# Kernel tuning notes

Measured on AMD Instinct MI355X. Metric: run time of the kernel, lower is better.

The kernel has to match this reference:

```python
import math
import jax, jax.numpy as jnp
import numpy as np

GROUPS = 32
EPS = 1e-5


def group_norm(x, w, b):
    # x: [B, C, H, W]
    B, C, H, W = x.shape
    xg = x.reshape(B, GROUPS, C // GROUPS, H, W)
    mean = xg.mean(axis=(2, 3, 4), keepdims=True)
    var = xg.var(axis=(2, 3, 4), keepdims=True)
    xg = (xg - mean) * jax.lax.rsqrt(var + EPS)
    x = xg.reshape(B, C, H, W)
    return x * w[None, :, None, None] + b[None, :, None, None]


def setup_inputs() -> dict:
    key = jax.random.key(0)
    ks = jax.random.split(key, 4)
    B, C, H, W = 16, 512, 32, 32
    x = jax.random.normal(ks[0], (B, C, H, W), dtype=jnp.float32)
    norm_w = jnp.ones((C,), dtype=jnp.float32)
    norm_b = jnp.zeros((C,), dtype=jnp.float32)
    qkv_w = jax.random.normal(ks[1], (3 * C, C), dtype=jnp.float32) / math.sqrt(C)
    qkv_b = jnp.zeros((3 * C,), dtype=jnp.float32)
    proj_w = jax.random.normal(ks[2], (C, C), dtype=jnp.float32) / math.sqrt(C)
    proj_b = jnp.zeros((C,), dtype=jnp.float32)
    return {"x": x, "norm_w": norm_w, "norm_b": norm_b,
            "qkv_w": qkv_w, "qkv_b": qkv_b,
            "proj_w": proj_w, "proj_b": proj_b}


def reference(x, norm_w, norm_b, qkv_w, qkv_b, proj_w, proj_b):
    B, C, H, W = x.shape
    xn = group_norm(x, norm_w, norm_b)
    # 1x1 conv == channel matmul: [B,3C,H,W]
    qkv = jnp.einsum('oc,bchw->bohw', qkv_w, xn) + qkv_b[None, :, None, None]
    q, k, v = jnp.split(qkv, 3, axis=1)
    q = q.reshape(B, C, H * W).transpose(0, 2, 1)  # [B, HW, C]
    k = k.reshape(B, C, H * W)                     # [B, C, HW]
    v = v.reshape(B, C, H * W).transpose(0, 2, 1)  # [B, HW, C]
    attn = jax.nn.softmax(jnp.einsum('bnc,bcm->bnm', q, k) / math.sqrt(C), axis=-1)
    h = jnp.einsum('bnm,bmc->bnc', attn, v)        # [B, HW, C]
    h = h.transpose(0, 2, 1).reshape(B, C, H, W)
    out = jnp.einsum('oc,bchw->bohw', proj_w, h) + proj_b[None, :, None, None]
    return out + x
```

## Files before the change

kernel.cpp:

```cpp
#include <hip/hip_runtime.h>

#define GLD16(gp, lp) __builtin_amdgcn_global_load_lds( \
    (const __attribute__((address_space(1))) void*)(gp), \
    (__attribute__((address_space(3))) void*)(lp), 16, 0, 0)

typedef __attribute__((ext_vector_type(8))) short bf16x8;
typedef __attribute__((ext_vector_type(4))) float f32x4;

__device__ __forceinline__ short f2bf(float f) {
    union { float f; unsigned u; } x; x.f = f;
    unsigned r = x.u + 0x7fffu + ((x.u >> 16) & 1u);
    return (short)(r >> 16);
}
__device__ __forceinline__ float bf2f(short s) {
    union { unsigned u; float f; } x;
    x.u = ((unsigned)(unsigned short)s) << 16;
    return x.f;
}

__global__ __launch_bounds__(256) void cvt_weights(
    const float* __restrict__ qkv_w, const float* __restrict__ proj_w,
    short* __restrict__ wq, short* __restrict__ wp)
{
    int idx = blockIdx.x * 256 + threadIdx.x;
    const int NQ4 = (1536 * 512) / 4;
    float4 f; short4 s;
    if (idx < NQ4) {
        f = ((const float4*)qkv_w)[idx];
        s.x = f2bf(f.x); s.y = f2bf(f.y); s.z = f2bf(f.z); s.w = f2bf(f.w);
        ((short4*)wq)[idx] = s;
    } else {
        int j = idx - NQ4;
        f = ((const float4*)proj_w)[j];
        s.x = f2bf(f.x); s.y = f2bf(f.y); s.z = f2bf(f.z); s.w = f2bf(f.w);
        ((short4*)wp)[j] = s;
    }
}

__global__ __launch_bounds__(256) void gn_stats(
    const float* __restrict__ x, float* __restrict__ mean, float* __restrict__ rstd)
{
    int bg = blockIdx.x;
    const float4* p = (const float4*)(x + (size_t)bg * 16384);
    float s = 0.f, ss = 0.f;
    for (int i = threadIdx.x; i < 4096; i += 256) {
        float4 v = p[i];
        s  += v.x + v.y + v.z + v.w;
        ss += v.x * v.x + v.y * v.y + v.z * v.z + v.w * v.w;
    }
    #pragma unroll
    for (int o = 32; o > 0; o >>= 1) {
        s  += __shfl_down(s, o);
        ss += __shfl_down(ss, o);
    }
    __shared__ float ls[4], lss[4];
    int wave = threadIdx.x >> 6;
    if ((threadIdx.x & 63) == 0) { ls[wave] = s; lss[wave] = ss; }
    __syncthreads();
    if (threadIdx.x == 0) {
        s  = ls[0] + ls[1] + ls[2] + ls[3];
        ss = lss[0] + lss[1] + lss[2] + lss[3];
        float m = s * (1.f / 16384.f);
        float var = ss * (1.f / 16384.f) - m * m;
        mean[bg] = m;
        rstd[bg] = rsqrtf(var + 1e-5f);
    }
}

__global__ __launch_bounds__(256) void gn_apply_t(
    const float* __restrict__ x, const float* __restrict__ w, const float* __restrict__ bb,
    const float* __restrict__ mean, const float* __restrict__ rstd,
    short* __restrict__ xnT)
{
    __shared__ short tile[64][65];
    int b = blockIdx.z, cblk = blockIdx.y, nblk = blockIdx.x;
    int t = threadIdx.x;
    int nl = t & 63;
    int cb = t >> 6;
    #pragma unroll
    for (int i = 0; i < 16; ++i) {
        int cl = cb * 16 + i;
        int cg = cblk * 64 + cl;
        int bgid = b * 32 + (cg >> 4);
        float sc = rstd[bgid] * w[cg];
        float sh = bb[cg] - mean[bgid] * sc;
        float xv = x[((size_t)(b * 512 + cg)) * 1024 + nblk * 64 + nl];
        tile[cl][nl] = f2bf(xv * sc + sh);
    }
    __syncthreads();
    int ng = t >> 4;
    int c4 = (t & 15) * 4;
    #pragma unroll
    for (int p = 0; p < 4; ++p) {
        int nl2 = p * 16 + ng;
        short4 sv;
        sv.x = tile[c4 + 0][nl2];
        sv.y = tile[c4 + 1][nl2];
        sv.z = tile[c4 + 2][nl2];
        sv.w = tile[c4 + 3][nl2];
        *(short4*)&xnT[((size_t)(b * 1024 + nblk * 64 + nl2)) * 512 + cblk * 64 + c4] = sv;
    }
}

__device__ __forceinline__ void gemm256(
    const short* __restrict__ A, const short* __restrict__ B,
    const int lda, const int ldb, const int NT,
    short* lds, f32x4 acc[8][4])
{
    const int tid  = threadIdx.x;
    const int lane = tid & 63;
    const int wave = tid >> 6;
    const int wm = wave >> 2;
    const int wn = wave & 3;
    const int fr = lane & 15;
    const int fk = lane >> 4;
    const int frx = fr & 7;

    const short* pa[4]; const short* pb[4];
    int la[4], lb[4];
    #pragma unroll
    for (int i = 0; i < 4; ++i) {
        int cid = i * 512 + tid;
        int row = cid >> 3;
        int sl  = cid & 7;
        int csw = sl ^ (row & 7);
        pa[i] = A + (size_t)row * lda + csw * 8;
        pb[i] = B + (size_t)row * ldb + csw * 8;
        la[i] = cid * 8;
        lb[i] = 16384 + cid * 8;
    }

    #pragma unroll
    for (int i = 0; i < 4; ++i) GLD16(pa[i], lds + la[i]);
    #pragma unroll
    for (int i = 0; i < 4; ++i) GLD16(pb[i], lds + lb[i]);
    #pragma unroll
    for (int i = 0; i < 4; ++i) { pa[i] += 64; pb[i] += 64; }

    const int arow0 = wm * 128 + fr;
    const int brow0 = wn * 64 + fr;
    const int slot0 = (fk ^ frx) << 3;
    const int slot1 = ((4 + fk) ^ frx) << 3;

    for (int t = 0; t < NT; ++t) {
        const int cur = (t & 1) << 15;
        const int nxt = 32768 - cur;
        const bool pre = (t + 1 < NT);

        if (pre) {
            #pragma unroll
            for (int i = 0; i < 4; ++i) GLD16(pa[i], lds + nxt + la[i]);
        }
        if (pre) asm volatile("s_waitcnt vmcnt(4)" ::: "memory");
        else     asm volatile("s_waitcnt vmcnt(0)" ::: "memory");
        asm volatile("s_barrier" ::: "memory");
        __builtin_amdgcn_sched_barrier(0);

        bf16x8 af[8], bfr[4];
        #pragma unroll
        for (int m = 0; m < 8; ++m)
            af[m] = *(const bf16x8*)&lds[cur + ((arow0 + m * 16) << 6) + slot0];
        #pragma unroll
        for (int n = 0; n < 4; ++n)
            bfr[n] = *(const bf16x8*)&lds[cur + 16384 + ((brow0 + n * 16) << 6) + slot0];
        if (pre) {
            #pragma unroll
            for (int i = 0; i < 4; ++i) GLD16(pb[i], lds + nxt + lb[i]);
        }
        __builtin_amdgcn_s_setprio(1);
        #pragma unroll
        for (int m = 0; m < 8; ++m)
            #pragma unroll
            for (int n = 0; n < 4; ++n)
                acc[m][n] = __builtin_amdgcn_mfma_f32_16x16x32_bf16(af[m], bfr[n], acc[m][n], 0, 0, 0);
        __builtin_amdgcn_s_setprio(0);

        #pragma unroll
        for (int m = 0; m < 8; ++m)
            af[m] = *(const bf16x8*)&lds[cur + ((arow0 + m * 16) << 6) + slot1];
        #pragma unroll
        for (int n = 0; n < 4; ++n)
            bfr[n] = *(const bf16x8*)&lds[cur + 16384 + ((brow0 + n * 16) << 6) + slot1];
        __builtin_amdgcn_s_setprio(1);
        #pragma unroll
        for (int m = 0; m < 8; ++m)
            #pragma unroll
            for (int n = 0; n < 4; ++n)
                acc[m][n] = __builtin_amdgcn_mfma_f32_16x16x32_bf16(af[m], bfr[n], acc[m][n], 0, 0, 0);
        __builtin_amdgcn_s_setprio(0);

        if (pre) {
            #pragma unroll
            for (int i = 0; i < 4; ++i) { pa[i] += 64; pb[i] += 64; }
        }
        asm volatile("s_barrier" ::: "memory");
        __builtin_amdgcn_sched_barrier(0);
    }
}

#define GEMM_EPI_IDX() \
    const int lane = threadIdx.x & 63; \
    const int wave = threadIdx.x >> 6; \
    const int wm = wave >> 2; \
    const int wn = wave & 3; \
    const int fq = lane >> 4; \
    const int fcol = lane & 15;

__global__ __launch_bounds__(512, 2) void qkv_gemm(
    const short* __restrict__ wq, const float* __restrict__ qkv_b,
    const short* __restrict__ xnT,
    short* __restrict__ qT, short* __restrict__ kT, short* __restrict__ vv)
{
    __shared__ short lds[65536];
    const int b = blockIdx.z, bm = blockIdx.y, bn = blockIdx.x;
    const short* A  = wq + (size_t)bm * 256 * 512;
    const short* Bb = xnT + ((size_t)b * 1024 + bn * 256) * 512;
    f32x4 acc[8][4];
    #pragma unroll
    for (int m = 0; m < 8; ++m)
        #pragma unroll
        for (int n = 0; n < 4; ++n) acc[m][n] = (f32x4){0.f, 0.f, 0.f, 0.f};
    gemm256(A, Bb, 512, 512, 8, lds, acc);

    GEMM_EPI_IDX();
    const int region = bm >> 1;
    const float qscale = 0.04419417382415922f;

    #pragma unroll
    for (int m = 0; m < 8; ++m) {
        int o0 = bm * 256 + wm * 128 + m * 16 + fq * 4;
        float4 bias = *(const float4*)&qkv_b[o0];
        float bb4[4] = {bias.x, bias.y, bias.z, bias.w};
        #pragma unroll
        for (int n = 0; n < 4; ++n) {
            int col = bn * 256 + wn * 64 + n * 16 + fcol;
            f32x4 a = acc[m][n];
            if (region == 0) {
                short4 sv;
                sv.x = f2bf((a[0] + bb4[0]) * qscale);
                sv.y = f2bf((a[1] + bb4[1]) * qscale);
                sv.z = f2bf((a[2] + bb4[2]) * qscale);
                sv.w = f2bf((a[3] + bb4[3]) * qscale);
                *(short4*)&qT[((size_t)(b * 1024 + col)) * 512 + o0] = sv;
            } else if (region == 1) {
                short4 sv;
                sv.x = f2bf(a[0] + bb4[0]);
                sv.y = f2bf(a[1] + bb4[1]);
                sv.z = f2bf(a[2] + bb4[2]);
                sv.w = f2bf(a[3] + bb4[3]);
                *(short4*)&kT[((size_t)(b * 1024 + col)) * 512 + (o0 - 512)] = sv;
            } else {
                #pragma unroll
                for (int r = 0; r < 4; ++r)
                    vv[((size_t)(b * 512 + (o0 - 1024 + r))) * 1024 + col] = f2bf(a[r] + bb4[r]);
            }
        }
    }
}

__global__ __launch_bounds__(512, 2) void s_gemm(
    const short* __restrict__ kT, const short* __restrict__ qT, short* __restrict__ S)
{
    __shared__ short lds[65536];
    const int b = blockIdx.z, bm = blockIdx.y, bn = blockIdx.x;
    const short* A  = kT + ((size_t)b * 1024 + bm * 256) * 512;
    const short* Bb = qT + ((size_t)b * 1024 + bn * 256) * 512;
    f32x4 acc[8][4];
    #pragma unroll
    for (int m = 0; m < 8; ++m)
        #pragma unroll
        for (int n = 0; n < 4; ++n) acc[m][n] = (f32x4){0.f, 0.f, 0.f, 0.f};
    gemm256(A, Bb, 512, 512, 8, lds, acc);

    GEMM_EPI_IDX();
    #pragma unroll
    for (int m = 0; m < 8; ++m) {
        int m0 = bm * 256 + wm * 128 + m * 16 + fq * 4;
        #pragma unroll
        for (int n = 0; n < 4; ++n) {
            int ncol = bn * 256 + wn * 64 + n * 16 + fcol;
            f32x4 a = acc[m][n];
            short4 sv;
            sv.x = f2bf(a[0]); sv.y = f2bf(a[1]); sv.z = f2bf(a[2]); sv.w = f2bf(a[3]);
            *(short4*)&S[((size_t)(b * 1024 + ncol)) * 1024 + m0] = sv;
        }
    }
}

__global__ __launch_bounds__(256) void softmax_rows(short* __restrict__ S)
{
    const int wave = threadIdx.x >> 6;
    const int lane = threadIdx.x & 63;
    size_t row = (size_t)blockIdx.x * 4 + wave;
    short* p = S + row * 1024;
    short4 raw[4];
    float v[16];
    #pragma unroll
    for (int i = 0; i < 4; ++i) raw[i] = ((short4*)p)[lane + 64 * i];
    #pragma unroll
    for (int i = 0; i < 4; ++i) {
        v[i * 4 + 0] = bf2f(raw[i].x);
        v[i * 4 + 1] = bf2f(raw[i].y);
        v[i * 4 + 2] = bf2f(raw[i].z);
        v[i * 4 + 3] = bf2f(raw[i].w);
    }
    float mx = v[0];
    #pragma unroll
    for (int i = 1; i < 16; ++i) mx = fmaxf(mx, v[i]);
    #pragma unroll
    for (int o = 1; o < 64; o <<= 1) mx = fmaxf(mx, __shfl_xor(mx, o));
    float sum = 0.f;
    #pragma unroll
    for (int i = 0; i < 16; ++i) { v[i] = __expf(v[i] - mx); sum += v[i]; }
    #pragma unroll
    for (int o = 1; o < 64; o <<= 1) sum += __shfl_xor(sum, o);
    float inv = 1.f / sum;
    #pragma unroll
    for (int i = 0; i < 4; ++i) {
        short4 sv;
        sv.x = f2bf(v[i * 4 + 0] * inv);
        sv.y = f2bf(v[i * 4 + 1] * inv);
        sv.z = f2bf(v[i * 4 + 2] * inv);
        sv.w = f2bf(v[i * 4 + 3] * inv);
        ((short4*)p)[lane + 64 * i] = sv;
    }
}

__global__ __launch_bounds__(512, 2) void pv_gemm(
    const short* __restrict__ vv, const short* __restrict__ P, short* __restrict__ h)
{
    __shared__ short lds[65536];
    const int b = blockIdx.z, bm = blockIdx.y, bn = blockIdx.x;
    const short* A  = vv + ((size_t)b * 512 + bm * 256) * 1024;
    const short* Bb = P + ((size_t)b * 1024 + bn * 256) * 1024;
    f32x4 acc[8][4];
    #pragma unroll
    for (int m = 0; m < 8; ++m)
        #pragma unroll
        for (int n = 0; n < 4; ++n) acc[m][n] = (f32x4){0.f, 0.f, 0.f, 0.f};
    gemm256(A, Bb, 1024, 1024, 16, lds, acc);

    GEMM_EPI_IDX();
    #pragma unroll
    for (int m = 0; m < 8; ++m) {
        int c0 = bm * 256 + wm * 128 + m * 16 + fq * 4;
        #pragma unroll
        for (int n = 0; n < 4; ++n) {
            int ncol = bn * 256 + wn * 64 + n * 16 + fcol;
            f32x4 a = acc[m][n];
            short4 sv;
            sv.x = f2bf(a[0]); sv.y = f2bf(a[1]); sv.z = f2bf(a[2]); sv.w = f2bf(a[3]);
            *(short4*)&h[((size_t)(b * 1024 + ncol)) * 512 + c0] = sv;
        }
    }
}

__global__ __launch_bounds__(512, 2) void proj_gemm(
    const short* __restrict__ wp, const float* __restrict__ proj_b,
    const short* __restrict__ h, const float* __restrict__ x, float* __restrict__ out)
{
    __shared__ short lds[65536];
    const int b = blockIdx.z, bm = blockIdx.y, bn = blockIdx.x;
    const short* A  = wp + (size_t)bm * 256 * 512;
    const short* Bb = h + ((size_t)b * 1024 + bn * 256) * 512;
    f32x4 acc[8][4];
    #pragma unroll
    for (int m = 0; m < 8; ++m)
        #pragma unroll
        for (int n = 0; n < 4; ++n) acc[m][n] = (f32x4){0.f, 0.f, 0.f, 0.f};
    gemm256(A, Bb, 512, 512, 8, lds, acc);

    GEMM_EPI_IDX();
    #pragma unroll
    for (int m = 0; m < 8; ++m) {
        int o0 = bm * 256 + wm * 128 + m * 16 + fq * 4;
        float4 pb = *(const float4*)&proj_b[o0];
        float pb4[4] = {pb.x, pb.y, pb.z, pb.w};
        #pragma unroll
        for (int n = 0; n < 4; ++n) {
            int col = bn * 256 + wn * 64 + n * 16 + fcol;
            f32x4 a = acc[m][n];
            #pragma unroll
            for (int r = 0; r < 4; ++r) {
                size_t idx = ((size_t)(b * 512 + o0 + r)) * 1024 + col;
                out[idx] = a[r] + pb4[r] + x[idx];
            }
        }
    }
}

extern "C" void kernel_launch(void* const* d_in, const int* in_sizes, int n_in,
                              void* d_out, int out_size, void* d_ws, size_t ws_size,
                              hipStream_t stream) {
    const float* x      = (const float*)d_in[0];
    const float* norm_w = (const float*)d_in[1];
    const float* norm_b = (const float*)d_in[2];
    const float* qkv_w  = (const float*)d_in[3];
    const float* qkv_b  = (const float*)d_in[4];
    const float* proj_w = (const float*)d_in[5];
    const float* proj_b = (const float*)d_in[6];
    float* out = (float*)d_out;

    char* ws = (char*)d_ws;
    size_t off = 0;
    auto alloc = [&](size_t bytes) {
        void* p = ws + off;
        off = (off + bytes + 255) & ~(size_t)255;
        return p;
    };
    float* mean = (float*)alloc(512 * 4);
    float* rstd = (float*)alloc(512 * 4);
    short* wq   = (short*)alloc((size_t)1536 * 512 * 2);
    short* wp   = (short*)alloc((size_t)512 * 512 * 2);
    short* xnT  = (short*)alloc((size_t)16 * 1024 * 512 * 2);
    short* qT   = (short*)alloc((size_t)16 * 1024 * 512 * 2);
    short* kT   = (short*)alloc((size_t)16 * 1024 * 512 * 2);
    short* vv   = (short*)alloc((size_t)16 * 512 * 1024 * 2);
    short* S    = (short*)alloc((size_t)16 * 1024 * 1024 * 2);
    short* h    = xnT;

    cvt_weights<<<1024, 256, 0, stream>>>(qkv_w, proj_w, wq, wp);
    gn_stats<<<512, 256, 0, stream>>>(x, mean, rstd);
    gn_apply_t<<<dim3(16, 8, 16), 256, 0, stream>>>(x, norm_w, norm_b, mean, rstd, xnT);
    qkv_gemm<<<dim3(4, 6, 16), 512, 0, stream>>>(wq, qkv_b, xnT, qT, kT, vv);
    s_gemm<<<dim3(4, 4, 16), 512, 0, stream>>>(kT, qT, S);
    softmax_rows<<<4096, 256, 0, stream>>>(S);
    pv_gemm<<<dim3(4, 2, 16), 512, 0, stream>>>(vv, S, h);
    proj_gemm<<<dim3(4, 2, 16), 512, 0, stream>>>(wp, proj_b, h, x, out);
}
```

Measured before the change: 247.3 us.

## Use 4-stage K=32 LDS pipeline and narrower N tiles for PV/proj GEMMs

Replaces the double-buffered K=64 GEMM mainloop with a templated 4-buffer pipeline using K=32 slices. It keeps three stages in flight, needs one barrier per iteration, and uses a new swizzle for 32-wide rows. PV and projection GEMMs switch to 128-wide N tiles with twice as many blocks, which should improve CU occupancy across 256 CUs. The cost is more loop iterations, more LDS fragment loads per MFMA, and a smaller tile that re-reads the A operand more often.

```diff
diff --git a/kernel.cpp b/kernel.cpp
--- a/kernel.cpp
+++ b/kernel.cpp
@@ -102,11 +102,14 @@
     }
 }
 
-__device__ __forceinline__ void gemm256(
+template<int NFR, int NT>
+__device__ __forceinline__ void gemm_core(
     const short* __restrict__ A, const short* __restrict__ B,
-    const int lda, const int ldb, const int NT,
-    short* lds, f32x4 acc[8][4])
-{
+    const int lda, const int ldb, short* lds, f32x4 acc[8][NFR])
+{
+    constexpr int BCH = NFR / 2;
+    constexpr int BUF = 8192 + NFR * 2048;
+    constexpr int LPS = 2 + BCH;
     const int tid  = threadIdx.x;
     const int lane = tid & 63;
     const int wave = tid >> 6;
@@ -114,104 +117,82 @@
     const int wn = wave & 3;
     const int fr = lane & 15;
     const int fk = lane >> 4;
-    const int frx = fr & 7;
-
-    const short* pa[4]; const short* pb[4];
-    int la[4], lb[4];
-    #pragma unroll
-    for (int i = 0; i < 4; ++i) {
+
+    const short* pa[2]; int la[2];
+    const short* pb[BCH]; int lb[BCH];
+    #pragma unroll
+    for (int i = 0; i < 2; ++i) {
         int cid = i * 512 + tid;
-        int row = cid >> 3;
-        int sl  = cid & 7;
-        int csw = sl ^ (row & 7);
+        int row = cid >> 2, sl = cid & 3;
+        int csw = sl ^ ((row >> 1) & 3);
         pa[i] = A + (size_t)row * lda + csw * 8;
+        la[i] = cid * 8;
+    }
+    #pragma unroll
+    for (int i = 0; i < BCH; ++i) {
+        int cid = i * 512 + tid;
+        int row = cid >> 2, sl = cid & 3;
+        int csw = sl ^ ((row >> 1) & 3);
         pb[i] = B + (size_t)row * ldb + csw * 8;
-        la[i] = cid * 8;
-        lb[i] = 16384 + cid * 8;
-    }
-
-    #pragma unroll
-    for (int i = 0; i < 4; ++i) GLD16(pa[i], lds + la[i]);
-    #pragma unroll
-    for (int i = 0; i < 4; ++i) GLD16(pb[i], lds + lb[i]);
-    #pragma unroll
-    for (int i = 0; i < 4; ++i) { pa[i] += 64; pb[i] += 64; }
+        lb[i] = 8192 + cid * 8;
+    }
+
+    auto stage = [&](int t) {
+        const int base = (t & 3) * BUF;
+        const int koff = t * 32;
+        #pragma unroll
+        for (int i = 0; i < 2; ++i) GLD16(pa[i] + koff, lds + base + la[i]);
+        #pragma unroll
+        for (int i = 0; i < BCH; ++i) GLD16(pb[i] + koff, lds + base + lb[i]);
+    };
+
+    stage(0); stage(1); stage(2);
+    asm volatile("s_waitcnt vmcnt(%0)" :: "n"(2 * LPS) : "memory");
+    asm volatile("s_barrier" ::: "memory");
 
     const int arow0 = wm * 128 + fr;
-    const int brow0 = wn * 64 + fr;
-    const int slot0 = (fk ^ frx) << 3;
-    const int slot1 = ((4 + fk) ^ frx) << 3;
+    const int brow0 = wn * (NFR * 16) + fr;
 
     for (int t = 0; t < NT; ++t) {
-        const int cur = (t & 1) << 15;
-        const int nxt = 32768 - cur;
-        const bool pre = (t + 1 < NT);
-
-        if (pre) {
-            #pragma unroll
-            for (int i = 0; i < 4; ++i) GLD16(pa[i], lds + nxt + la[i]);
-        }
-        if (pre) asm volatile("s_waitcnt vmcnt(4)" ::: "memory");
-        else     asm volatile("s_waitcnt vmcnt(0)" ::: "memory");
-        asm volatile("s_barrier" ::: "memory");
-        __builtin_amdgcn_sched_barrier(0);
-
-        bf16x8 af[8], bfr[4];
-        #pragma unroll
-        for (int m = 0; m < 8; ++m)
-            af[m] = *(const bf16x8*)&lds[cur + ((arow0 + m * 16) << 6) + slot0];
-        #pragma unroll
-        for (int n = 0; n < 4; ++n)
-            bfr[n] = *(const bf16x8*)&lds[cur + 16384 + ((brow0 + n * 16) << 6) + slot0];
-        if (pre) {
-            #pragma unroll
-            for (int i = 0; i < 4; ++i) GLD16(pb[i], lds + nxt + lb[i]);
+        const int base = (t & 3) * BUF;
+        bf16x8 af[8], bfr[NFR];
+        #pragma unroll
+        for (int m = 0; m < 8; ++m) {
+            int R = arow0 + m * 16;
+            af[m] = *(const bf16x8*)&lds[base + R * 32 + ((fk ^ ((R >> 1) & 3)) << 3)];
+        }
+        #pragma unroll
+        for (int n = 0; n < NFR; ++n) {
+            int R = brow0 + n * 16;
+            bfr[n] = *(const bf16x8*)&lds[base + 8192 + R * 32 + ((fk ^ ((R >> 1) & 3)) << 3)];
         }
         __builtin_amdgcn_s_setprio(1);
         #pragma unroll
         for (int m = 0; m < 8; ++m)
             #pragma unroll
-            for (int n = 0; n < 4; ++n)
+            for (int n = 0; n < NFR; ++n)
                 acc[m][n] = __builtin_amdgcn_mfma_f32_16x16x32_bf16(af[m], bfr[n], acc[m][n], 0, 0, 0);
         __builtin_amdgcn_s_setprio(0);
 
-        #pragma unroll
-        for (int m = 0; m < 8; ++m)
-            af[m] = *(const bf16x8*)&lds[cur + ((arow0 + m * 16) << 6) + slot1];
-        #pragma unroll
-        for (int n = 0; n < 4; ++n)
-            bfr[n] = *(const bf16x8*)&lds[cur + 16384 + ((brow0 + n * 16) << 6) + slot1];
-        __builtin_amdgcn_s_setprio(1);
-        #pragma unroll
-        for (int m = 0; m < 8; ++m)
-            #pragma unroll
-            for (int n = 0; n < 4; ++n)
-                acc[m][n] = __builtin_amdgcn_mfma_f32_16x16x32_bf16(af[m], bfr[n], acc[m][n], 0, 0, 0);
-        __builtin_amdgcn_s_setprio(0);
-
-        if (pre) {
-            #pragma unroll
-            for (int i = 0; i < 4; ++i) { pa[i] += 64; pb[i] += 64; }
-        }
-        asm volatile("s_barrier" ::: "memory");
-        __builtin_amdgcn_sched_barrier(0);
-    }
-}
-
-#define GEMM_EPI_IDX() \
-    const int lane = threadIdx.x & 63; \
-    const int wave = threadIdx.x >> 6; \
-    const int wm = wave >> 2; \
-    const int wn = wave & 3; \
-    const int fq = lane >> 4; \
-    const int fcol = lane & 15;
+        if (t + 3 < NT) stage(t + 3);
+        if (t + 1 < NT) {
+            if (t + 3 < NT)
+                asm volatile("s_waitcnt vmcnt(%0)" :: "n"(2 * LPS) : "memory");
+            else if (t + 2 < NT)
+                asm volatile("s_waitcnt vmcnt(%0)" :: "n"(LPS) : "memory");
+            else
+                asm volatile("s_waitcnt vmcnt(0)" ::: "memory");
+            asm volatile("s_barrier" ::: "memory");
+        }
+    }
+}
 
 __global__ __launch_bounds__(512, 2) void qkv_gemm(
     const short* __restrict__ wq, const float* __restrict__ qkv_b,
     const short* __restrict__ xnT,
     short* __restrict__ qT, short* __restrict__ kT, short* __restrict__ vv)
 {
-    __shared__ short lds[65536];
+    __shared__ short lds[4 * (8192 + 4 * 2048)];
     const int b = blockIdx.z, bm = blockIdx.y, bn = blockIdx.x;
     const short* A  = wq + (size_t)bm * 256 * 512;
     const short* Bb = xnT + ((size_t)b * 1024 + bn * 256) * 512;
@@ -220,9 +201,12 @@
     for (int m = 0; m < 8; ++m)
         #pragma unroll
         for (int n = 0; n < 4; ++n) acc[m][n] = (f32x4){0.f, 0.f, 0.f, 0.f};
-    gemm256(A, Bb, 512, 512, 8, lds, acc);
-
-    GEMM_EPI_IDX();
+    gemm_core<4, 16>(A, Bb, 512, 512, lds, acc);
+
+    const int lane = threadIdx.x & 63;
+    const int wave = threadIdx.x >> 6;
+    const int wm = wave >> 2, wn = wave & 3;
+    const int fq = lane >> 4, fcol = lane & 15;
     const int region = bm >> 1;
     const float qscale = 0.04419417382415922f;
 
@@ -261,7 +245,7 @@
 __global__ __launch_bounds__(512, 2) void s_gemm(
     const short* __restrict__ kT, const short* __restrict__ qT, short* __restrict__ S)
 {
-    __shared__ short lds[65536];
+    __shared__ short lds[4 * (8192 + 4 * 2048)];
     const int b = blockIdx.z, bm = blockIdx.y, bn = blockIdx.x;
     const short* A  = kT + ((size_t)b * 1024 + bm * 256) * 512;
     const short* Bb = qT + ((size_t)b * 1024 + bn * 256) * 512;
@@ -270,9 +254,12 @@
     for (int m = 0; m < 8; ++m)
         #pragma unroll
         for (int n = 0; n < 4; ++n) acc[m][n] = (f32x4){0.f, 0.f, 0.f, 0.f};
-    gemm256(A, Bb, 512, 512, 8, lds, acc);
-
-    GEMM_EPI_IDX();
+    gemm_core<4, 16>(A, Bb, 512, 512, lds, acc);
+
+    const int lane = threadIdx.x & 63;
+    const int wave = threadIdx.x >> 6;
+    const int wm = wave >> 2, wn = wave & 3;
+    const int fq = lane >> 4, fcol = lane & 15;
     #pragma unroll
     for (int m = 0; m < 8; ++m) {
         int m0 = bm * 256 + wm * 128 + m * 16 + fq * 4;
@@ -329,24 +316,27 @@
 __global__ __launch_bounds__(512, 2) void pv_gemm(
     const short* __restrict__ vv, const short* __restrict__ P, short* __restrict__ h)
 {
-    __shared__ short lds[65536];
+    __shared__ short lds[4 * (8192 + 2 * 2048)];
     const int b = blockIdx.z, bm = blockIdx.y, bn = blockIdx.x;
     const short* A  = vv + ((size_t)b * 512 + bm * 256) * 1024;
-    const short* Bb = P + ((size_t)b * 1024 + bn * 256) * 1024;
-    f32x4 acc[8][4];
+    const short* Bb = P + ((size_t)b * 1024 + bn * 128) * 1024;
+    f32x4 acc[8][2];
     #pragma unroll
     for (int m = 0; m < 8; ++m)
         #pragma unroll
-        for (int n = 0; n < 4; ++n) acc[m][n] = (f32x4){0.f, 0.f, 0.f, 0.f};
-    gemm256(A, Bb, 1024, 1024, 16, lds, acc);
-
-    GEMM_EPI_IDX();
+        for (int n = 0; n < 2; ++n) acc[m][n] = (f32x4){0.f, 0.f, 0.f, 0.f};
+    gemm_core<2, 32>(A, Bb, 1024, 1024, lds, acc);
+
+    const int lane = threadIdx.x & 63;
+    const int wave = threadIdx.x >> 6;
+    const int wm = wave >> 2, wn = wave & 3;
+    const int fq = lane >> 4, fcol = lane & 15;
     #pragma unroll
     for (int m = 0; m < 8; ++m) {
         int c0 = bm * 256 + wm * 128 + m * 16 + fq * 4;
         #pragma unroll
-        for (int n = 0; n < 4; ++n) {
-            int ncol = bn * 256 + wn * 64 + n * 16 + fcol;
+        for (int n = 0; n < 2; ++n) {
+            int ncol = bn * 128 + wn * 32 + n * 16 + fcol;
             f32x4 a = acc[m][n];
             short4 sv;
             sv.x = f2bf(a[0]); sv.y = f2bf(a[1]); sv.z = f2bf(a[2]); sv.w = f2bf(a[3]);
@@ -359,26 +349,29 @@
     const short* __restrict__ wp, const float* __restrict__ proj_b,
     const short* __restrict__ h, const float* __restrict__ x, float* __restrict__ out)
 {
-    __shared__ short lds[65536];
+    __shared__ short lds[4 * (8192 + 2 * 2048)];
     const int b = blockIdx.z, bm = blockIdx.y, bn = blockIdx.x;
     const short* A  = wp + (size_t)bm * 256 * 512;
-    const short* Bb = h + ((size_t)b * 1024 + bn * 256) * 512;
-    f32x4 acc[8][4];
+    const short* Bb = h + ((size_t)b * 1024 + bn * 128) * 512;
+    f32x4 acc[8][2];
     #pragma unroll
     for (int m = 0; m < 8; ++m)
         #pragma unroll
-        for (int n = 0; n < 4; ++n) acc[m][n] = (f32x4){0.f, 0.f, 0.f, 0.f};
-    gemm256(A, Bb, 512, 512, 8, lds, acc);
-
-    GEMM_EPI_IDX();
+        for (int n = 0; n < 2; ++n) acc[m][n] = (f32x4){0.f, 0.f, 0.f, 0.f};
+    gemm_core<2, 16>(A, Bb, 512, 512, lds, acc);
+
+    const int lane = threadIdx.x & 63;
+    const int wave = threadIdx.x >> 6;
+    const int wm = wave >> 2, wn = wave & 3;
+    const int fq = lane >> 4, fcol = lane & 15;
     #pragma unroll
     for (int m = 0; m < 8; ++m) {
         int o0 = bm * 256 + wm * 128 + m * 16 + fq * 4;
         float4 pb = *(const float4*)&proj_b[o0];
         float pb4[4] = {pb.x, pb.y, pb.z, pb.w};
         #pragma unroll
-        for (int n = 0; n < 4; ++n) {
-            int col = bn * 256 + wn * 64 + n * 16 + fcol;
+        for (int n = 0; n < 2; ++n) {
+            int col = bn * 128 + wn * 32 + n * 16 + fcol;
             f32x4 a = acc[m][n];
             #pragma unroll
             for (int r = 0; r < 4; ++r) {
@@ -425,6 +418,6 @@
     qkv_gemm<<<dim3(4, 6, 16), 512, 0, stream>>>(wq, qkv_b, xnT, qT, kT, vv);
     s_gemm<<<dim3(4, 4, 16), 512, 0, stream>>>(kT, qT, S);
     softmax_rows<<<4096, 256, 0, stream>>>(S);
-    pv_gemm<<<dim3(4, 2, 16), 512, 0, stream>>>(vv, S, h);
-    proj_gemm<<<dim3(4, 2, 16), 512, 0, stream>>>(wp, proj_b, h, x, out);
-}
+    pv_gemm<<<dim3(8, 2, 16), 512, 0, stream>>>(vv, S, h);
+    proj_gemm<<<dim3(8, 2, 16), 512, 0, stream>>>(wp, proj_b, h, x, out);
+}
```

Measured after the change: 243.1 us. About the same (-1.7%).

## Use triple-buffered K32 GEMM pipeline, XCD-aware block swizzle, and fuse prep kernels

Applied to the files above, without the earlier changes.

Rewrites the shared GEMM mainloop to use K=32 stages in a three-slot LDS ring (96KB instead of 128KB) with a new XOR swizzle. Loads are issued two stages ahead and B fragment reads are split around interleaved barriers, so global-load latency overlaps MFMA work. All GEMM launches become 1D grids remapped so that neighbouring tiles land on the same XCD, which should improve L2 reuse. Weight conversion and group-norm statistics are merged into a single launch. The cost is more barriers per K step and higher scheduling complexity.

```diff
diff --git a/kernel.cpp b/kernel.cpp
--- a/kernel.cpp
+++ b/kernel.cpp
@@ -17,53 +17,55 @@
     x.u = ((unsigned)(unsigned short)s) << 16;
     return x.f;
 }
-
-__global__ __launch_bounds__(256) void cvt_weights(
+__device__ __forceinline__ int xcd_swz(int id, int n) {
+    return (id & 7) * (n >> 3) + (id >> 3);
+}
+
+__global__ __launch_bounds__(256) void prep(
     const float* __restrict__ qkv_w, const float* __restrict__ proj_w,
-    short* __restrict__ wq, short* __restrict__ wp)
-{
-    int idx = blockIdx.x * 256 + threadIdx.x;
-    const int NQ4 = (1536 * 512) / 4;
-    float4 f; short4 s;
-    if (idx < NQ4) {
-        f = ((const float4*)qkv_w)[idx];
-        s.x = f2bf(f.x); s.y = f2bf(f.y); s.z = f2bf(f.z); s.w = f2bf(f.w);
-        ((short4*)wq)[idx] = s;
+    short* __restrict__ wq, short* __restrict__ wp,
+    const float* __restrict__ x, float* __restrict__ mean, float* __restrict__ rstd)
+{
+    if (blockIdx.x < 1024) {
+        int idx = blockIdx.x * 256 + threadIdx.x;
+        const int NQ4 = (1536 * 512) / 4;
+        float4 f; short4 s;
+        if (idx < NQ4) {
+            f = ((const float4*)qkv_w)[idx];
+            s.x = f2bf(f.x); s.y = f2bf(f.y); s.z = f2bf(f.z); s.w = f2bf(f.w);
+            ((short4*)wq)[idx] = s;
+        } else {
+            int j = idx - NQ4;
+            f = ((const float4*)proj_w)[j];
+            s.x = f2bf(f.x); s.y = f2bf(f.y); s.z = f2bf(f.z); s.w = f2bf(f.w);
+            ((short4*)wp)[j] = s;
+        }
     } else {
-        int j = idx - NQ4;
-        f = ((const float4*)proj_w)[j];
-        s.x = f2bf(f.x); s.y = f2bf(f.y); s.z = f2bf(f.z); s.w = f2bf(f.w);
-        ((short4*)wp)[j] = s;
-    }
-}
-
-__global__ __launch_bounds__(256) void gn_stats(
-    const float* __restrict__ x, float* __restrict__ mean, float* __restrict__ rstd)
-{
-    int bg = blockIdx.x;
-    const float4* p = (const float4*)(x + (size_t)bg * 16384);
-    float s = 0.f, ss = 0.f;
-    for (int i = threadIdx.x; i < 4096; i += 256) {
-        float4 v = p[i];
-        s  += v.x + v.y + v.z + v.w;
-        ss += v.x * v.x + v.y * v.y + v.z * v.z + v.w * v.w;
-    }
-    #pragma unroll
-    for (int o = 32; o > 0; o >>= 1) {
-        s  += __shfl_down(s, o);
-        ss += __shfl_down(ss, o);
-    }
-    __shared__ float ls[4], lss[4];
-    int wave = threadIdx.x >> 6;
-    if ((threadIdx.x & 63) == 0) { ls[wave] = s; lss[wave] = ss; }
-    __syncthreads();
-    if (threadIdx.x == 0) {
-        s  = ls[0] + ls[1] + ls[2] + ls[3];
-        ss = lss[0] + lss[1] + lss[2] + lss[3];
-        float m = s * (1.f / 16384.f);
-        float var = ss * (1.f / 16384.f) - m * m;
-        mean[bg] = m;
-        rstd[bg] = rsqrtf(var + 1e-5f);
+        int bg = blockIdx.x - 1024;
+        const float4* p = (const float4*)(x + (size_t)bg * 16384);
+        float s = 0.f, ss = 0.f;
+        for (int i = threadIdx.x; i < 4096; i += 256) {
+            float4 v = p[i];
+            s  += v.x + v.y + v.z + v.w;
+            ss += v.x * v.x + v.y * v.y + v.z * v.z + v.w * v.w;
+        }
+        #pragma unroll
+        for (int o = 32; o > 0; o >>= 1) {
+            s  += __shfl_down(s, o);
+            ss += __shfl_down(ss, o);
+        }
+        __shared__ float ls[4], lss[4];
+        int wave = threadIdx.x >> 6;
+        if ((threadIdx.x & 63) == 0) { ls[wave] = s; lss[wave] = ss; }
+        __syncthreads();
+        if (threadIdx.x == 0) {
+            s  = ls[0] + ls[1] + ls[2] + ls[3];
+            ss = lss[0] + lss[1] + lss[2] + lss[3];
+            float m = s * (1.f / 16384.f);
+            float var = ss * (1.f / 16384.f) - m * m;
+            mean[bg] = m;
+            rstd[bg] = rsqrtf(var + 1e-5f);
+        }
     }
 }
 
@@ -102,10 +104,10 @@
     }
 }
 
-__device__ __forceinline__ void gemm256(
+template<int NT>
+__device__ __forceinline__ void gemm256_8p(
     const short* __restrict__ A, const short* __restrict__ B,
-    const int lda, const int ldb, const int NT,
-    short* lds, f32x4 acc[8][4])
+    const int lda, const int ldb, short* lds, f32x4 acc[8][4])
 {
     const int tid  = threadIdx.x;
     const int lane = tid & 63;
@@ -114,91 +116,93 @@
     const int wn = wave & 3;
     const int fr = lane & 15;
     const int fk = lane >> 4;
-    const int frx = fr & 7;
-
-    const short* pa[4]; const short* pb[4];
-    int la[4], lb[4];
-    #pragma unroll
-    for (int i = 0; i < 4; ++i) {
+
+    const short* pa[2]; const short* pb[2]; int la[2], lb[2];
+    #pragma unroll
+    for (int i = 0; i < 2; ++i) {
         int cid = i * 512 + tid;
-        int row = cid >> 3;
-        int sl  = cid & 7;
-        int csw = sl ^ (row & 7);
+        int row = cid >> 2, sl = cid & 3;
+        int csw = sl ^ ((row >> 1) & 3);
         pa[i] = A + (size_t)row * lda + csw * 8;
         pb[i] = B + (size_t)row * ldb + csw * 8;
         la[i] = cid * 8;
-        lb[i] = 16384 + cid * 8;
-    }
-
-    #pragma unroll
-    for (int i = 0; i < 4; ++i) GLD16(pa[i], lds + la[i]);
-    #pragma unroll
-    for (int i = 0; i < 4; ++i) GLD16(pb[i], lds + lb[i]);
-    #pragma unroll
-    for (int i = 0; i < 4; ++i) { pa[i] += 64; pb[i] += 64; }
+        lb[i] = 8192 + cid * 8;
+    }
+
+    #pragma unroll
+    for (int i = 0; i < 2; ++i) GLD16(pa[i],      lds + la[i]);
+    #pragma unroll
+    for (int i = 0; i < 2; ++i) GLD16(pb[i],      lds + lb[i]);
+    #pragma unroll
+    for (int i = 0; i < 2; ++i) GLD16(pa[i] + 32, lds + 16384 + la[i]);
+    #pragma unroll
+    for (int i = 0; i < 2; ++i) GLD16(pb[i] + 32, lds + 16384 + lb[i]);
+    asm volatile("s_waitcnt vmcnt(4)" ::: "memory");
+    asm volatile("s_barrier" ::: "memory");
 
     const int arow0 = wm * 128 + fr;
     const int brow0 = wn * 64 + fr;
-    const int slot0 = (fk ^ frx) << 3;
-    const int slot1 = ((4 + fk) ^ frx) << 3;
-
+
+    int base = 0, sbase = 32768, kst = 64;
     for (int t = 0; t < NT; ++t) {
-        const int cur = (t & 1) << 15;
-        const int nxt = 32768 - cur;
-        const bool pre = (t + 1 < NT);
+        const short* lA = lds + base;
+        const short* lB = lds + base + 8192;
+        const bool pre = (t + 2 < NT);
 
         if (pre) {
+            GLD16(pa[0] + kst, lds + sbase + la[0]);
+            GLD16(pa[1] + kst, lds + sbase + la[1]);
+        }
+        bf16x8 af[8], bf0[2];
+        #pragma unroll
+        for (int m = 0; m < 8; ++m) {
+            int R = arow0 + m * 16;
+            af[m] = *(const bf16x8*)&lA[R * 32 + ((fk ^ ((R >> 1) & 3)) << 3)];
+        }
+        #pragma unroll
+        for (int n = 0; n < 2; ++n) {
+            int R = brow0 + n * 16;
+            bf0[n] = *(const bf16x8*)&lB[R * 32 + ((fk ^ ((R >> 1) & 3)) << 3)];
+        }
+        asm volatile("s_barrier" ::: "memory");
+        __builtin_amdgcn_s_setprio(1);
+        #pragma unroll
+        for (int m = 0; m < 8; ++m)
             #pragma unroll
-            for (int i = 0; i < 4; ++i) GLD16(pa[i], lds + nxt + la[i]);
-        }
-        if (pre) asm volatile("s_waitcnt vmcnt(4)" ::: "memory");
-        else     asm volatile("s_waitcnt vmcnt(0)" ::: "memory");
+            for (int n = 0; n < 2; ++n)
+                acc[m][n] = __builtin_amdgcn_mfma_f32_16x16x32_bf16(af[m], bf0[n], acc[m][n], 0, 0, 0);
+        __builtin_amdgcn_s_setprio(0);
+
+        if (pre) {
+            GLD16(pb[0] + kst, lds + sbase + lb[0]);
+            GLD16(pb[1] + kst, lds + sbase + lb[1]);
+        }
+        bf16x8 bf1[2];
+        #pragma unroll
+        for (int n = 0; n < 2; ++n) {
+            int R = brow0 + (n + 2) * 16;
+            bf1[n] = *(const bf16x8*)&lB[R * 32 + ((fk ^ ((R >> 1) & 3)) << 3)];
+        }
+        asm volatile("s_barrier" ::: "memory");
+        __builtin_amdgcn_s_setprio(1);
+        #pragma unroll
+        for (int m = 0; m < 8; ++m)
+            #pragma unroll
+            for (int n = 0; n < 2; ++n)
+                acc[m][n + 2] = __builtin_amdgcn_mfma_f32_16x16x32_bf16(af[m], bf1[n], acc[m][n + 2], 0, 0, 0);
+        __builtin_amdgcn_s_setprio(0);
+
+        if (pre)                 asm volatile("s_waitcnt vmcnt(4)" ::: "memory");
+        else if (t + 1 < NT)     asm volatile("s_waitcnt vmcnt(0)" ::: "memory");
         asm volatile("s_barrier" ::: "memory");
         __builtin_amdgcn_sched_barrier(0);
-
-        bf16x8 af[8], bfr[4];
-        #pragma unroll
-        for (int m = 0; m < 8; ++m)
-            af[m] = *(const bf16x8*)&lds[cur + ((arow0 + m * 16) << 6) + slot0];
-        #pragma unroll
-        for (int n = 0; n < 4; ++n)
-            bfr[n] = *(const bf16x8*)&lds[cur + 16384 + ((brow0 + n * 16) << 6) + slot0];
-        if (pre) {
-            #pragma unroll
-            for (int i = 0; i < 4; ++i) GLD16(pb[i], lds + nxt + lb[i]);
-        }
-        __builtin_amdgcn_s_setprio(1);
-        #pragma unroll
-        for (int m = 0; m < 8; ++m)
-            #pragma unroll
-            for (int n = 0; n < 4; ++n)
-                acc[m][n] = __builtin_amdgcn_mfma_f32_16x16x32_bf16(af[m], bfr[n], acc[m][n], 0, 0, 0);
-        __builtin_amdgcn_s_setprio(0);
-
-        #pragma unroll
-        for (int m = 0; m < 8; ++m)
-            af[m] = *(const bf16x8*)&lds[cur + ((arow0 + m * 16) << 6) + slot1];
-        #pragma unroll
-        for (int n = 0; n < 4; ++n)
-            bfr[n] = *(const bf16x8*)&lds[cur + 16384 + ((brow0 + n * 16) << 6) + slot1];
-        __builtin_amdgcn_s_setprio(1);
-        #pragma unroll
-        for (int m = 0; m < 8; ++m)
-            #pragma unroll
-            for (int n = 0; n < 4; ++n)
-                acc[m][n] = __builtin_amdgcn_mfma_f32_16x16x32_bf16(af[m], bfr[n], acc[m][n], 0, 0, 0);
-        __builtin_amdgcn_s_setprio(0);
-
-        if (pre) {
-            #pragma unroll
-            for (int i = 0; i < 4; ++i) { pa[i] += 64; pb[i] += 64; }
-        }
-        asm volatile("s_barrier" ::: "memory");
-        __builtin_amdgcn_sched_barrier(0);
-    }
-}
-
-#define GEMM_EPI_IDX() \
+        base  = (base  == 32768) ? 0 : base  + 16384;
+        sbase = (sbase == 32768) ? 0 : sbase + 16384;
+        kst += 32;
+    }
+}
+
+#define EPI_IDX() \
     const int lane = threadIdx.x & 63; \
     const int wave = threadIdx.x >> 6; \
     const int wm = wave >> 2; \
@@ -211,8 +215,9 @@
     const short* __restrict__ xnT,
     short* __restrict__ qT, short* __restrict__ kT, short* __restrict__ vv)
 {
-    __shared__ short lds[65536];
-    const int b = blockIdx.z, bm = blockIdx.y, bn = blockIdx.x;
+    __shared__ short lds[49152];
+    int wg = xcd_swz(blockIdx.x, 384);
+    const int bn = wg & 3, bm = (wg >> 2) % 6, b = wg / 24;
     const short* A  = wq + (size_t)bm * 256 * 512;
     const short* Bb = xnT + ((size_t)b * 1024 + bn * 256) * 512;
     f32x4 acc[8][4];
@@ -220,9 +225,9 @@
     for (int m = 0; m < 8; ++m)
         #pragma unroll
         for (int n = 0; n < 4; ++n) acc[m][n] = (f32x4){0.f, 0.f, 0.f, 0.f};
-    gemm256(A, Bb, 512, 512, 8, lds, acc);
-
-    GEMM_EPI_IDX();
+    gemm256_8p<16>(A, Bb, 512, 512, lds, acc);
+
+    EPI_IDX();
     const int region = bm >> 1;
     const float qscale = 0.04419417382415922f;
 
@@ -261,8 +266,9 @@
 __global__ __launch_bounds__(512, 2) void s_gemm(
     const short* __restrict__ kT, const short* __restrict__ qT, short* __restrict__ S)
 {
-    __shared__ short lds[65536];
-    const int b = blockIdx.z, bm = blockIdx.y, bn = blockIdx.x;
+    __shared__ short lds[49152];
+    int wg = xcd_swz(blockIdx.x, 256);
+    const int bn = wg & 3, bm = (wg >> 2) & 3, b = wg >> 4;
     const short* A  = kT + ((size_t)b * 1024 + bm * 256) * 512;
     const short* Bb = qT + ((size_t)b * 1024 + bn * 256) * 512;
     f32x4 acc[8][4];
@@ -270,9 +276,9 @@
     for (int m = 0; m < 8; ++m)
         #pragma unroll
         for (int n = 0; n < 4; ++n) acc[m][n] = (f32x4){0.f, 0.f, 0.f, 0.f};
-    gemm256(A, Bb, 512, 512, 8, lds, acc);
-
-    GEMM_EPI_IDX();
+    gemm256_8p<16>(A, Bb, 512, 512, lds, acc);
+
+    EPI_IDX();
     #pragma unroll
     for (int m = 0; m < 8; ++m) {
         int m0 = bm * 256 + wm * 128 + m * 16 + fq * 4;
@@ -329,8 +335,9 @@
 __global__ __launch_bounds__(512, 2) void pv_gemm(
     const short* __restrict__ vv, const short* __restrict__ P, short* __restrict__ h)
 {
-    __shared__ short lds[65536];
-    const int b = blockIdx.z, bm = blockIdx.y, bn = blockIdx.x;
+    __shared__ short lds[49152];
+    int wg = xcd_swz(blockIdx.x, 128);
+    const int bn = wg & 3, bm = (wg >> 2) & 1, b = wg >> 3;
     const short* A  = vv + ((size_t)b * 512 + bm * 256) * 1024;
     const short* Bb = P + ((size_t)b * 1024 + bn * 256) * 1024;
     f32x4 acc[8][4];
@@ -338,9 +345,9 @@
     for (int m = 0; m < 8; ++m)
         #pragma unroll
         for (int n = 0; n < 4; ++n) acc[m][n] = (f32x4){0.f, 0.f, 0.f, 0.f};
-    gemm256(A, Bb, 1024, 1024, 16, lds, acc);
-
-    GEMM_EPI_IDX();
+    gemm256_8p<32>(A, Bb, 1024, 1024, lds, acc);
+
+    EPI_IDX();
     #pragma unroll
     for (int m = 0; m < 8; ++m) {
         int c0 = bm * 256 + wm * 128 + m * 16 + fq * 4;
@@ -359,8 +366,9 @@
     const short* __restrict__ wp, const float* __restrict__ proj_b,
     const short* __restrict__ h, const float* __restrict__ x, float* __restrict__ out)
 {
-    __shared__ short lds[65536];
-    const int b = blockIdx.z, bm = blockIdx.y, bn = blockIdx.x;
+    __shared__ short lds[49152];
+    int wg = xcd_swz(blockIdx.x, 128);
+    const int bn = wg & 3, bm = (wg >> 2) & 1, b = wg >> 3;
     const short* A  = wp + (size_t)bm * 256 * 512;
     const short* Bb = h + ((size_t)b * 1024 + bn * 256) * 512;
     f32x4 acc[8][4];
@@ -368,9 +376,9 @@
     for (int m = 0; m < 8; ++m)
         #pragma unroll
         for (int n = 0; n < 4; ++n) acc[m][n] = (f32x4){0.f, 0.f, 0.f, 0.f};
-    gemm256(A, Bb, 512, 512, 8, lds, acc);
-
-    GEMM_EPI_IDX();
+    gemm256_8p<16>(A, Bb, 512, 512, lds, acc);
+
+    EPI_IDX();
     #pragma unroll
     for (int m = 0; m < 8; ++m) {
         int o0 = bm * 256 + wm * 128 + m * 16 + fq * 4;
@@ -419,12 +427,11 @@
     short* S    = (short*)alloc((size_t)16 * 1024 * 1024 * 2);
     short* h    = xnT;
 
-    cvt_weights<<<1024, 256, 0, stream>>>(qkv_w, proj_w, wq, wp);
-    gn_stats<<<512, 256, 0, stream>>>(x, mean, rstd);
+    prep<<<1536, 256, 0, stream>>>(qkv_w, proj_w, wq, wp, x, mean, rstd);
     gn_apply_t<<<dim3(16, 8, 16), 256, 0, stream>>>(x, norm_w, norm_b, mean, rstd, xnT);
-    qkv_gemm<<<dim3(4, 6, 16), 512, 0, stream>>>(wq, qkv_b, xnT, qT, kT, vv);
-    s_gemm<<<dim3(4, 4, 16), 512, 0, stream>>>(kT, qT, S);
+    qkv_gemm<<<384, 512, 0, stream>>>(wq, qkv_b, xnT, qT, kT, vv);
+    s_gemm<<<256, 512, 0, stream>>>(kT, qT, S);
     softmax_rows<<<4096, 256, 0, stream>>>(S);
-    pv_gemm<<<dim3(4, 2, 16), 512, 0, stream>>>(vv, S, h);
-    proj_gemm<<<dim3(4, 2, 16), 512, 0, stream>>>(wp, proj_b, h, x, out);
-}
+    pv_gemm<<<128, 512, 0, stream>>>(vv, S, h);
+    proj_gemm<<<128, 512, 0, stream>>>(wp, proj_b, h, x, out);
+}
```

New measurement: 243.1 us. Within noise of the previous version (-1.7%).
